# Kernel optimization log

Hardware: AMD Instinct MI355X
Metric: run time of the kernel (lower is better)

Reference implementation:

```python
import jax, jax.numpy as jnp
import numpy as np

K = 20  # neighbors per point (module default)


def _knn_idx(x, k):
    # x: [N, d] -> indices of k nearest points (self included, as in torch_cluster.knn)
    d2 = jnp.sum(x * x, axis=-1)
    dist = d2[:, None] + d2[None, :] - 2.0 * (x @ x.T)  # [N, N] squared distances
    _, idx = jax.lax.top_k(-dist, k)  # smallest distances
    return idx  # [N, k]


def _mlp(h, layers):
    # layers: list of (W, b, relu_flag); BN is identity (eval mode, fresh running stats)
    for W, b, relu in layers:
        h = h @ W + b
        if relu:
            h = jax.nn.relu(h)
    return h


def _dynamic_edge_conv(x, layers, k=K):
    # x: [B, N, d]; dynamic kNN graph per graph, edge feat [x_i, x_j - x_i], MLP, max-aggr
    idx = jax.vmap(lambda xx: _knn_idx(jax.lax.stop_gradient(xx), k))(x)  # [B, N, k]
    xj = jax.vmap(lambda xx, ii: xx[ii])(x, idx)  # [B, N, k, d] neighbor gather
    xi = x[:, :, None, :]
    feat = jnp.concatenate([jnp.broadcast_to(xi, xj.shape), xj - xi], axis=-1)  # [B,N,k,2d]
    return jnp.max(_mlp(feat, layers), axis=2)  # [B, N, d_out]


def setup_inputs() -> dict:
    key = jax.random.key(0)
    ks = jax.random.split(key, 20)
    s = 0.05
    B, N, PD, OUT = 8, 4096, 2, 10
    f32 = jnp.float32

    def w(k, shape):
        return jax.random.normal(k, shape, dtype=f32) * s

    return {
        "data": jax.random.normal(ks[0], (B, N, PD), dtype=f32),
        # conv1 MLP: [2*PD, 64, 64, 64]
        "c1w1": w(ks[1], (2 * PD, 64)), "c1b1": jnp.zeros((64,), f32),
        "c1w2": w(ks[2], (64, 64)),     "c1b2": jnp.zeros((64,), f32),
        "c1w3": w(ks[3], (64, 64)),     "c1b3": jnp.zeros((64,), f32),
        # conv2 MLP: [2*64, 128]
        "c2w1": w(ks[4], (128, 128)),   "c2b1": jnp.zeros((128,), f32),
        # lin1: 192 -> 1024
        "lin1_w": w(ks[5], (192, 1024)), "lin1_b": jnp.zeros((1024,), f32),
        # head MLP: [1024, 512, 256, OUT]
        "mw1": w(ks[6], (1024, 512)), "mb1": jnp.zeros((512,), f32),
        "mw2": w(ks[7], (512, 256)),  "mb2": jnp.zeros((256,), f32),
        "mw3": w(ks[8], (256, OUT)),  "mb3": jnp.zeros((OUT,), f32),
    }


def reference(data, c1w1, c1b1, c1w2, c1b2, c1w3, c1b3, c2w1, c2b1,
              lin1_w, lin1_b, mw1, mb1, mw2, mb2, mw3, mb3):
    # DynamicEdgeConv 1: MLP([4,64,64,64]) (plain last layer)
    x1 = _dynamic_edge_conv(data, [(c1w1, c1b1, True), (c1w2, c1b2, True), (c1w3, c1b3, False)])
    # DynamicEdgeConv 2: MLP([128,128]) (single plain linear)
    x2 = _dynamic_edge_conv(x1, [(c2w1, c2b1, False)])
    out = jnp.concatenate([x1, x2], axis=-1) @ lin1_w + lin1_b  # [B, N, 1024]
    out = jnp.max(out, axis=1)  # global max pool over points -> [B, 1024]
    out = _mlp(out, [(mw1, mb1, True), (mw2, mb2, True), (mw3, mb3, False)])
    return jax.nn.log_softmax(out, axis=1)
```

## Files before the change

### kernel.cpp

```cpp
#include <hip/hip_runtime.h>
#include <math.h>

#define DEVI static __device__ __forceinline__
#define F_INF __builtin_inff()

DEVI bool lexlt(float d, int i, float dr, int ir)
{
    return (d < dr) || (d == dr && i < ir);
}

DEVI void insert20(float* bd, int* bi, float d, int i)
{
#pragma unroll
    for (int j = 19; j >= 1; --j) {
        bool lt  = d < bd[j];
        bool ltp = d < bd[j - 1];
        float nd = ltp ? bd[j - 1] : d;
        int   ni = ltp ? bi[j - 1] : i;
        bd[j] = lt ? nd : bd[j];
        bi[j] = lt ? ni : bi[j];
    }
    bool lt0 = d < bd[0];
    bd[0] = lt0 ? d : bd[0];
    bi[0] = lt0 ? i : bi[0];
}

DEVI void insert_tiered(float* bd, int* bi, float d, int i)
{
    if (__all(!(d < bd[15]))) {
#pragma unroll
        for (int j = 19; j >= 17; --j) {
            bool lt  = d < bd[j];
            bool ltp = d < bd[j - 1];
            float nd = ltp ? bd[j - 1] : d;
            int   ni = ltp ? bi[j - 1] : i;
            bd[j] = lt ? nd : bd[j];
            bi[j] = lt ? ni : bi[j];
        }
        bool lt16 = d < bd[16];
        bd[16] = lt16 ? d : bd[16];
        bi[16] = lt16 ? i : bi[16];
    } else if (__all(!(d < bd[7]))) {
#pragma unroll
        for (int j = 19; j >= 9; --j) {
            bool lt  = d < bd[j];
            bool ltp = d < bd[j - 1];
            float nd = ltp ? bd[j - 1] : d;
            int   ni = ltp ? bi[j - 1] : i;
            bd[j] = lt ? nd : bd[j];
            bi[j] = lt ? ni : bi[j];
        }
        bool lt8 = d < bd[8];
        bd[8] = lt8 ? d : bd[8];
        bi[8] = lt8 ? i : bi[8];
    } else {
        insert20(bd, bi, d, i);
    }
}

DEVI void flushT(float* bd, int* bi, float d, int i, int e, int cnt)
{
    bool want = (e < cnt) && (d < bd[19]);
    if (__any(want))
        insert_tiered(bd, bi, want ? d : F_INF, want ? i : 0x7FFFFFFF);
}

#define FLUSH() do { \
    flushT(bd, bi, a0, j0, 0, cnt); \
    flushT(bd, bi, a1, j1, 1, cnt); \
    flushT(bd, bi, a2, j2, 2, cnt); \
    flushT(bd, bi, a3, j3, 3, cnt); \
    cnt = 0; thr = bd[19]; \
} while (0)

#define APPEND(dv, civ) do { \
    bool pass_ = (dv) < thr; \
    if (pass_) { \
        a0 = (cnt == 0) ? (dv) : a0; j0 = (cnt == 0) ? (civ) : j0; \
        a1 = (cnt == 1) ? (dv) : a1; j1 = (cnt == 1) ? (civ) : j1; \
        a2 = (cnt == 2) ? (dv) : a2; j2 = (cnt == 2) ? (civ) : j2; \
        a3 = (cnt == 3) ? (dv) : a3; j3 = (cnt == 3) ? (civ) : j3; \
        ++cnt; \
    } \
    if (__any(cnt == 4)) { FLUSH(); } \
} while (0)

__global__ __launch_bounds__(256) void k_merge8(const float* __restrict__ partD,
                                                const int* __restrict__ partI,
                                                int* __restrict__ idxo)
{
    int q = blockIdx.x * 256 + threadIdx.x;
    const float* rd = partD + (size_t)q * 160;
    const int*   ri = partI + (size_t)q * 160;
    int p0 = 0, p1 = 0, p2 = 0, p3 = 0, p4 = 0, p5 = 0, p6 = 0, p7 = 0;
    int* op = idxo + (size_t)q * 20;
    for (int r = 0; r < 20; ++r) {
        float d0 = rd[p0],        d1 = rd[20 + p1];
        float d2v = rd[40 + p2],  d3 = rd[60 + p3];
        float d4 = rd[80 + p4],   d5 = rd[100 + p5];
        float d6 = rd[120 + p6],  d7 = rd[140 + p7];
        int   i0 = ri[p0],        i1 = ri[20 + p1];
        int   i2 = ri[40 + p2],   i3 = ri[60 + p3];
        int   i4v = ri[80 + p4],  i5 = ri[100 + p5];
        int   i6 = ri[120 + p6],  i7 = ri[140 + p7];
        bool wA = lexlt(d1, i1, d0, i0);   float dA = wA ? d1 : d0; int iA = wA ? i1 : i0; int sA = wA ? 1 : 0;
        bool wB = lexlt(d3, i3, d2v, i2);  float dB = wB ? d3 : d2v; int iB = wB ? i3 : i2; int sB = wB ? 3 : 2;
        bool wC = lexlt(d5, i5, d4, i4v);  float dC = wC ? d5 : d4; int iC = wC ? i5 : i4v; int sC = wC ? 5 : 4;
        bool wD = lexlt(d7, i7, d6, i6);   float dD = wD ? d7 : d6; int iD = wD ? i7 : i6; int sD = wD ? 7 : 6;
        bool wE = lexlt(dB, iB, dA, iA);   float dE = wE ? dB : dA; int iE = wE ? iB : iA; int sE = wE ? sB : sA;
        bool wF = lexlt(dD, iD, dC, iC);   float dF = wF ? dD : dC; int iF = wF ? iD : iC; int sF = wF ? sD : sC;
        bool wG = lexlt(dF, iF, dE, iE);   int ig = wG ? iF : iE;   int sg = wG ? sF : sE;
        op[r] = ig;
        p0 += (sg == 0); p1 += (sg == 1); p2 += (sg == 2); p3 += (sg == 3);
        p4 += (sg == 4); p5 += (sg == 5); p6 += (sg == 6); p7 += (sg == 7);
    }
}

__global__ __launch_bounds__(256, 4) void k_knn2d(const float* __restrict__ x,
                                                  float* __restrict__ partD, int* __restrict__ partI)
{
    __shared__ float2 pts[4096];
    int t = threadIdx.x;
    int blk = blockIdx.x;
    int b = blk >> 7;
    int qt = (blk >> 1) & 63;
    int s = blk & 1;
    const float* xb = x + (size_t)b * 4096 * 2;
    for (int f = t; f < 2048; f += 256)
        ((float4*)pts)[f] = ((const float4*)xb)[f];
    __syncthreads();

    int l = t & 63, w = t >> 6;
    int q = qt * 64 + l;
    float2 qp = pts[q];
    float d2i = qp.x * qp.x + qp.y * qp.y;

    float bd[20]; int bi[20];
#pragma unroll
    for (int j = 0; j < 20; ++j) { bd[j] = F_INF; bi[j] = -1; }
    int cnt = 0; float thr = F_INF;
    float a0 = 0, a1 = 0, a2 = 0, a3 = 0;
    int   j0 = 0, j1 = 0, j2 = 0, j3 = 0;

    int m0 = s * 2048 + w * 512;
    for (int m = m0; m < m0 + 512; ++m) {
        float2 p = pts[m];
        float d2j = p.x * p.x + p.y * p.y;
        float dot = qp.x * p.x + qp.y * p.y;
        float dist = (d2i + d2j) - 2.0f * dot;
        APPEND(dist, m);
    }
    FLUSH();

    size_t base = (((size_t)(b * 4096 + q)) * 8 + s * 4 + w) * 20;
#pragma unroll
    for (int k = 0; k < 20; ++k) { partD[base + k] = bd[k]; partI[base + k] = bi[k]; }
}

__global__ void k_prep1(const float* __restrict__ x, const float* __restrict__ w1,
                        const float* __restrict__ b1, float* __restrict__ pm, float* __restrict__ qv)
{
    int tid = blockIdx.x * 256 + threadIdx.x;
    int n = tid >> 6, i = tid & 63;
    float x0 = x[(size_t)n * 2], x1v = x[(size_t)n * 2 + 1];
    float wa = w1[i], wb = w1[64 + i], wc = w1[128 + i], wd = w1[192 + i];
    pm[tid] = fmaf(x0, wa - wc, fmaf(x1v, wb - wd, b1[i]));
    qv[tid] = fmaf(x0, wc, x1v * wd);
}

__global__ __launch_bounds__(256) void k_edge1(const float* __restrict__ pm, const float* __restrict__ q,
                                               const int* __restrict__ idx1,
                                               const float* __restrict__ w2, const float* __restrict__ b2,
                                               const float* __restrict__ w3, const float* __restrict__ b3,
                                               float* __restrict__ x1, float* __restrict__ d2x1)
{
    int t = threadIdx.x;
    int w = t >> 6, l = t & 63;
    int pg = l / 20;
    int k  = l - pg * 20;
    int n0 = blockIdx.x * 12 + w * 3 + pg;
    bool valid = (l < 60) && (n0 < 32768);
    int n = valid ? n0 : 0;
    int b = n >> 12;
    int j = idx1[(size_t)n * 20 + k];
    const float4* pmr = (const float4*)(pm + (size_t)n * 64);
    const float4* qr  = (const float4*)(q + ((size_t)(b * 4096) + j) * 64);

    float h1[64];
#pragma unroll
    for (int i4 = 0; i4 < 16; ++i4) {
        float4 a = pmr[i4], c = qr[i4];
        h1[i4 * 4 + 0] = fmaxf(a.x + c.x, 0.f);
        h1[i4 * 4 + 1] = fmaxf(a.y + c.y, 0.f);
        h1[i4 * 4 + 2] = fmaxf(a.z + c.z, 0.f);
        h1[i4 * 4 + 3] = fmaxf(a.w + c.w, 0.f);
    }
    float h2[64];
#pragma unroll
    for (int o = 0; o < 64; ++o) h2[o] = b2[o];
#pragma unroll
    for (int i = 0; i < 64; ++i) {
        const float* r = w2 + i * 64;
#pragma unroll
        for (int o = 0; o < 64; ++o) h2[o] = fmaf(h1[i], r[o], h2[o]);
    }
#pragma unroll
    for (int o = 0; o < 64; ++o) h2[o] = fmaxf(h2[o], 0.f);

    float h3[64];
#pragma unroll
    for (int o = 0; o < 64; ++o) h3[o] = b3[o];
#pragma unroll
    for (int i = 0; i < 64; ++i) {
        const float* r = w3 + i * 64;
#pragma unroll
        for (int o = 0; o < 64; ++o) h3[o] = fmaf(h2[i], r[o], h3[o]);
    }

    int s16 = (k + 16 < 20) ? (l + 16) : l;
    int s8  = (k + 8  < 20) ? (l + 8)  : l;
    int s4  = (k + 4  < 20) ? (l + 4)  : l;
    int s2  = (k + 2  < 20) ? (l + 2)  : l;
    int s1  = (k + 1  < 20) ? (l + 1)  : l;
#pragma unroll
    for (int o = 0; o < 64; ++o) {
        float v = h3[o];
        v = fmaxf(v, __shfl(v, s16));
        v = fmaxf(v, __shfl(v, s8));
        v = fmaxf(v, __shfl(v, s4));
        v = fmaxf(v, __shfl(v, s2));
        v = fmaxf(v, __shfl(v, s1));
        h3[o] = v;
    }
    if (valid && k == 0) {
        float d2 = 0.f;
#pragma unroll
        for (int o = 0; o < 64; ++o) d2 += h3[o] * h3[o];
        float4* op = (float4*)(x1 + (size_t)n * 64);
#pragma unroll
        for (int i4 = 0; i4 < 16; ++i4)
            op[i4] = make_float4(h3[i4 * 4], h3[i4 * 4 + 1], h3[i4 * 4 + 2], h3[i4 * 4 + 3]);
        d2x1[n] = d2;
    }
}

#define S68 68
__global__ __launch_bounds__(256, 4) void k_knn64(const float* __restrict__ x1,
                                                  const float* __restrict__ d2x1,
                                                  float* __restrict__ partD, int* __restrict__ partI)
{
    __shared__ float smem[2 * 64 * S68 + 128];
    float* Qs   = smem;
    float* Cs   = smem + 64 * S68;
    float* d2q  = smem + 2 * 64 * S68;
    float* d2cs = d2q + 64;

    int t  = threadIdx.x;
    int blk = blockIdx.x;
    int bb = blk >> 7;
    int qt = (blk >> 1) & 63;
    int s  = blk & 1;
    int qbase  = bb * 4096 + qt * 64;
    int cstart = s * 2048;

    for (int f = t; f < 1024; f += 256) {
        int qq = f >> 4, dp = f & 15;
        *(float4*)&Qs[qq * S68 + dp * 4] =
            *(const float4*)(x1 + ((size_t)(qbase + qq)) * 64 + dp * 4);
    }
    if (t < 64) d2q[t] = d2x1[qbase + t];
    __syncthreads();

    int w = t >> 6, l = t & 63;
    int m = l & 15, p = l >> 4;
    float* Crow = Cs + (16 * w) * S68;

    float bd[20]; int bi[20];
#pragma unroll
    for (int j = 0; j < 20; ++j) { bd[j] = F_INF; bi[j] = -1; }
    int cnt = 0; float thr = F_INF;
    float a0 = 0, a1 = 0, a2 = 0, a3 = 0;
    int   j0 = 0, j1 = 0, j2 = 0, j3 = 0;

    float d2qr[4];
#pragma unroll
    for (int i = 0; i < 4; ++i) d2qr[i] = d2q[m + 16 * i];

    for (int T = 0; T < 32; ++T) {
        int cg = bb * 4096 + cstart + T * 64 + 16 * w;

#pragma unroll
        for (int r = 0; r < 4; ++r) {
            int rl = 4 * r + p;
            *(float4*)&Crow[rl * S68 + m * 4] =
                *(const float4*)(x1 + ((size_t)(cg + rl)) * 64 + m * 4);
        }
        if (l < 16) d2cs[16 * w + l] = d2x1[cg + l];

        float acc[4][4];
#pragma unroll
        for (int i = 0; i < 4; ++i)
#pragma unroll
            for (int j = 0; j < 4; ++j) acc[i][j] = 0.f;
#pragma unroll
        for (int dc = 0; dc < 16; ++dc) {
            float4 qv[4], cv[4];
#pragma unroll
            for (int i = 0; i < 4; ++i) qv[i] = *(const float4*)&Qs[(m + 16 * i) * S68 + dc * 4];
#pragma unroll
            for (int j = 0; j < 4; ++j) cv[j] = *(const float4*)&Crow[(4 * p + j) * S68 + dc * 4];
#pragma unroll
            for (int i = 0; i < 4; ++i)
#pragma unroll
                for (int j = 0; j < 4; ++j) {
                    acc[i][j] = fmaf(qv[i].x, cv[j].x, acc[i][j]);
                    acc[i][j] = fmaf(qv[i].y, cv[j].y, acc[i][j]);
                    acc[i][j] = fmaf(qv[i].z, cv[j].z, acc[i][j]);
                    acc[i][j] = fmaf(qv[i].w, cv[j].w, acc[i][j]);
                }
        }
        float d2cr[4];
#pragma unroll
        for (int j = 0; j < 4; ++j) d2cr[j] = d2cs[16 * w + 4 * p + j];

#pragma unroll
        for (int j = 0; j < 4; ++j)
#pragma unroll
            for (int i = 0; i < 4; ++i)
                Crow[(4 * p + j) * S68 + (m + 16 * i)] =
                    (d2qr[i] + d2cr[j]) - 2.0f * acc[i][j];

        int cib = cstart + T * 64 + 16 * w;
#pragma unroll
        for (int c = 0; c < 16; ++c) {
            float dv = Crow[c * S68 + l];
            APPEND(dv, cib + c);
        }
    }
    FLUSH();

    size_t base = (((size_t)(qbase + l)) * 8 + s * 4 + w) * 20;
#pragma unroll
    for (int k = 0; k < 20; ++k) { partD[base + k] = bd[k]; partI[base + k] = bi[k]; }
}

__global__ __launch_bounds__(128) void k_prep2(const float* __restrict__ x1, const float* __restrict__ w,
                                               const float* __restrict__ bias,
                                               float* __restrict__ T, float* __restrict__ V)
{
    __shared__ float xs[8][64];
    int o = threadIdx.x;
    int g = blockIdx.x * 8;
    for (int t = threadIdx.x; t < 512; t += 128) xs[t >> 6][t & 63] = x1[(size_t)g * 64 + t];
    __syncthreads();
    float at[8] = {}, av[8] = {};
    for (int i = 0; i < 64; ++i) {
        float wt = w[i * 128 + o], wv = w[(64 + i) * 128 + o];
#pragma unroll
        for (int p = 0; p < 8; ++p) {
            float xv = xs[p][i];
            at[p] = fmaf(xv, wt, at[p]);
            av[p] = fmaf(xv, wv, av[p]);
        }
    }
    float bo = bias[o];
#pragma unroll
    for (int p = 0; p < 8; ++p) {
        T[(size_t)(g + p) * 128 + o] = at[p] - av[p] + bo;
        V[(size_t)(g + p) * 128 + o] = av[p];
    }
}

__global__ __launch_bounds__(256) void k_edge2(const float* __restrict__ T, const float* __restrict__ V,
                                               const int* __restrict__ idx2, float* __restrict__ x2)
{
    int t = threadIdx.x;
    int p = t >> 5, oc = t & 31;
    int n = blockIdx.x * 8 + p;
    int b = n >> 12;
    const int* ip = idx2 + (size_t)n * 20;
    float4 mx = make_float4(-F_INF, -F_INF, -F_INF, -F_INF);
    for (int k = 0; k < 20; ++k) {
        int j = ip[k];
        float4 v = ((const float4*)(V + ((size_t)(b * 4096) + j) * 128))[oc];
        mx.x = fmaxf(mx.x, v.x); mx.y = fmaxf(mx.y, v.y);
        mx.z = fmaxf(mx.z, v.z); mx.w = fmaxf(mx.w, v.w);
    }
    float4 tv = ((const float4*)(T + (size_t)n * 128))[oc];
    float4 r = make_float4(tv.x + mx.x, tv.y + mx.y, tv.z + mx.z, tv.w + mx.w);
    ((float4*)(x2 + (size_t)n * 128))[oc] = r;
}

__global__ __launch_bounds__(256) void k_lin1max(const float* __restrict__ x1, const float* __restrict__ x2,
                                                 const float* __restrict__ w, const float* __restrict__ bias,
                                                 float* __restrict__ partial)
{
    __shared__ float fs[32][192];
    int blk = blockIdx.x;
    int b = blk >> 7, c = blk & 127;
    int base_n = b * 4096 + c * 32;
    for (int t = threadIdx.x; t < 2048; t += 256) {
        int n = t >> 6, i = t & 63;
        fs[n][i] = x1[(size_t)(base_n + n) * 64 + i];
    }
    for (int t = threadIdx.x; t < 4096; t += 256) {
        int n = t >> 7, i = t & 127;
        fs[n][64 + i] = x2[(size_t)(base_n + n) * 128 + i];
    }
    __syncthreads();

    float acc[32][4];
#pragma unroll
    for (int n = 0; n < 32; ++n)
#pragma unroll
        for (int oo = 0; oo < 4; ++oo) acc[n][oo] = 0.f;

    for (int i4 = 0; i4 < 48; ++i4) {
        float wv[4][4];
#pragma unroll
        for (int r = 0; r < 4; ++r)
#pragma unroll
            for (int oo = 0; oo < 4; ++oo)
                wv[r][oo] = w[(size_t)(i4 * 4 + r) * 1024 + oo * 256 + threadIdx.x];
#pragma unroll
        for (int n = 0; n < 32; ++n) {
            float4 f = *(const float4*)&fs[n][i4 * 4];
#pragma unroll
            for (int oo = 0; oo < 4; ++oo) {
                acc[n][oo] = fmaf(f.x, wv[0][oo], acc[n][oo]);
                acc[n][oo] = fmaf(f.y, wv[1][oo], acc[n][oo]);
                acc[n][oo] = fmaf(f.z, wv[2][oo], acc[n][oo]);
                acc[n][oo] = fmaf(f.w, wv[3][oo], acc[n][oo]);
            }
        }
    }
#pragma unroll
    for (int oo = 0; oo < 4; ++oo) {
        int o = oo * 256 + threadIdx.x;
        float m = -F_INF;
#pragma unroll
        for (int n = 0; n < 32; ++n) m = fmaxf(m, acc[n][oo]);
        partial[((size_t)b * 128 + c) * 1024 + o] = m + bias[o];
    }
}

__global__ void k_red(const float* __restrict__ partial, float* __restrict__ pooled)
{
    int t = blockIdx.x * 256 + threadIdx.x;
    int b = t >> 10, o = t & 1023;
    float m = -F_INF;
    for (int c = 0; c < 128; ++c) m = fmaxf(m, partial[((size_t)b * 128 + c) * 1024 + o]);
    pooled[t] = m;
}

__global__ __launch_bounds__(256) void k_fc1(const float* __restrict__ pooled, const float* __restrict__ w,
                                             const float* __restrict__ bias, float* __restrict__ g1)
{
    __shared__ float ps[8 * 1024];
    for (int t = threadIdx.x; t < 8192; t += 256) ps[t] = pooled[t];
    __syncthreads();
    int o = blockIdx.x * 256 + threadIdx.x;
    float acc[8] = {};
    for (int i4 = 0; i4 < 256; ++i4) {
        float w0 = w[(size_t)(i4 * 4 + 0) * 512 + o];
        float w1v = w[(size_t)(i4 * 4 + 1) * 512 + o];
        float w2v = w[(size_t)(i4 * 4 + 2) * 512 + o];
        float w3v = w[(size_t)(i4 * 4 + 3) * 512 + o];
#pragma unroll
        for (int bb = 0; bb < 8; ++bb) {
            float4 f = *(const float4*)&ps[bb * 1024 + i4 * 4];
            acc[bb] = fmaf(f.x, w0, fmaf(f.y, w1v, fmaf(f.z, w2v, fmaf(f.w, w3v, acc[bb]))));
        }
    }
    float bo = bias[o];
#pragma unroll
    for (int bb = 0; bb < 8; ++bb) g1[bb * 512 + o] = fmaxf(acc[bb] + bo, 0.f);
}

__global__ __launch_bounds__(256) void k_fc2(const float* __restrict__ g1, const float* __restrict__ w,
                                             const float* __restrict__ bias, float* __restrict__ g2)
{
    __shared__ float gs[8 * 512];
    for (int t = threadIdx.x; t < 4096; t += 256) gs[t] = g1[t];
    __syncthreads();
    int o = threadIdx.x;
    float acc[8] = {};
    for (int i4 = 0; i4 < 128; ++i4) {
        float w0 = w[(size_t)(i4 * 4 + 0) * 256 + o];
        float w1v = w[(size_t)(i4 * 4 + 1) * 256 + o];
        float w2v = w[(size_t)(i4 * 4 + 2) * 256 + o];
        float w3v = w[(size_t)(i4 * 4 + 3) * 256 + o];
#pragma unroll
        for (int bb = 0; bb < 8; ++bb) {
            float4 f = *(const float4*)&gs[bb * 512 + i4 * 4];
            acc[bb] = fmaf(f.x, w0, fmaf(f.y, w1v, fmaf(f.z, w2v, fmaf(f.w, w3v, acc[bb]))));
        }
    }
    float bo = bias[o];
#pragma unroll
    for (int bb = 0; bb < 8; ++bb) g2[bb * 256 + o] = fmaxf(acc[bb] + bo, 0.f);
}

__global__ void k_fc3sm(const float* __restrict__ g2, const float* __restrict__ w,
                        const float* __restrict__ bias, float* __restrict__ out)
{
    int t = threadIdx.x;
    int b = t >> 4, l = t & 15;
    float lg = -F_INF;
    if (l < 10) {
        float a = bias[l];
        for (int i = 0; i < 256; ++i) a = fmaf(g2[b * 256 + i], w[i * 10 + l], a);
        lg = a;
    }
    float m = lg;
    m = fmaxf(m, __shfl_xor(m, 1, 16));
    m = fmaxf(m, __shfl_xor(m, 2, 16));
    m = fmaxf(m, __shfl_xor(m, 4, 16));
    m = fmaxf(m, __shfl_xor(m, 8, 16));
    float e = (l < 10) ? expf(lg - m) : 0.f;
    float s = e;
    s += __shfl_xor(s, 1, 16);
    s += __shfl_xor(s, 2, 16);
    s += __shfl_xor(s, 4, 16);
    s += __shfl_xor(s, 8, 16);
    if (l < 10) out[b * 10 + l] = (lg - m) - logf(s);
}

extern "C" void kernel_launch(void* const* d_in, const int* in_sizes, int n_in,
                              void* d_out, int out_size, void* d_ws, size_t ws_size,
                              hipStream_t stream)
{
    (void)in_sizes; (void)n_in; (void)out_size; (void)ws_size;
    const float* data  = (const float*)d_in[0];
    const float* c1w1  = (const float*)d_in[1];
    const float* c1b1  = (const float*)d_in[2];
    const float* c1w2  = (const float*)d_in[3];
    const float* c1b2  = (const float*)d_in[4];
    const float* c1w3  = (const float*)d_in[5];
    const float* c1b3  = (const float*)d_in[6];
    const float* c2w1  = (const float*)d_in[7];
    const float* c2b1  = (const float*)d_in[8];
    const float* lin1w = (const float*)d_in[9];
    const float* lin1b = (const float*)d_in[10];
    const float* mw1   = (const float*)d_in[11];
    const float* mb1   = (const float*)d_in[12];
    const float* mw2   = (const float*)d_in[13];
    const float* mb2   = (const float*)d_in[14];
    const float* mw3   = (const float*)d_in[15];
    const float* mb3   = (const float*)d_in[16];
    float* ws  = (float*)d_ws;
    int*   wsi = (int*)d_ws;
    float* out = (float*)d_out;

    const size_t OFF_IDX1 = 0;
    const size_t OFF_IDX2 = 0;
    const size_t OFF_X1   = 655360;
    const size_t OFF_D2   = 2752512;
    const size_t OFF_PM   = 2785280;
    const size_t OFF_Q    = 4882432;
    const size_t OFF_PD   = 2785280;
    const size_t OFF_PI   = 8028160;
    const size_t OFF_T    = 2785280;
    const size_t OFF_V    = 6979584;
    const size_t OFF_X2   = 11173888;
    const size_t OFF_PART = 15368192;
    const size_t OFF_POOL = 16416768;
    const size_t OFF_G1   = 16424960;
    const size_t OFF_G2   = 16429056;

    k_knn2d<<<1024, 256, 0, stream>>>(data, ws + OFF_PD, wsi + OFF_PI);
    k_merge8<<<128, 256, 0, stream>>>(ws + OFF_PD, wsi + OFF_PI, wsi + OFF_IDX1);
    k_prep1<<<8192, 256, 0, stream>>>(data, c1w1, c1b1, ws + OFF_PM, ws + OFF_Q);
    k_edge1<<<2731, 256, 0, stream>>>(ws + OFF_PM, ws + OFF_Q, wsi + OFF_IDX1,
                                      c1w2, c1b2, c1w3, c1b3, ws + OFF_X1, ws + OFF_D2);
    k_knn64<<<1024, 256, 0, stream>>>(ws + OFF_X1, ws + OFF_D2, ws + OFF_PD, wsi + OFF_PI);
    k_merge8<<<128, 256, 0, stream>>>(ws + OFF_PD, wsi + OFF_PI, wsi + OFF_IDX2);
    k_prep2<<<4096, 128, 0, stream>>>(ws + OFF_X1, c2w1, c2b1, ws + OFF_T, ws + OFF_V);
    k_edge2<<<4096, 256, 0, stream>>>(ws + OFF_T, ws + OFF_V, wsi + OFF_IDX2, ws + OFF_X2);
    k_lin1max<<<1024, 256, 0, stream>>>(ws + OFF_X1, ws + OFF_X2, lin1w, lin1b, ws + OFF_PART);
    k_red<<<32, 256, 0, stream>>>(ws + OFF_PART, ws + OFF_POOL);
    k_fc1<<<2, 256, 0, stream>>>(ws + OFF_POOL, mw1, mb1, ws + OFF_G1);
    k_fc2<<<1, 256, 0, stream>>>(ws + OFF_G1, mw2, mb2, ws + OFF_G2);
    k_fc3sm<<<1, 128, 0, stream>>>(ws + OFF_G2, mw3, mb3, out);
}
```

Measured before the change: 1.445 ms.

## Hold query rows in registers and stream candidates as scalar loads in knn64

The 64-dim kNN kernel drops the shared-memory register-tiled 4x4 dot-product micro-kernel. Each thread now keeps its own query row in 64 registers and reads each candidate row through a wave-uniform (readfirstlane) pointer, so candidate data comes in as scalar/broadcast loads with no LDS staging or distance transpose. This removes the LDS traffic and the shared scratch, but puts much higher register pressure on each thread and gives up the 4x4 reuse of loaded operands. The merge kernel also moves from 256-thread to 64-thread blocks, giving more blocks for the same query count.

```diff
diff --git a/kernel.cpp b/kernel.cpp
--- a/kernel.cpp
+++ b/kernel.cpp
@@ -85,11 +85,11 @@
     if (__any(cnt == 4)) { FLUSH(); } \
 } while (0)
 
-__global__ __launch_bounds__(256) void k_merge8(const float* __restrict__ partD,
-                                                const int* __restrict__ partI,
-                                                int* __restrict__ idxo)
-{
-    int q = blockIdx.x * 256 + threadIdx.x;
+__global__ __launch_bounds__(64) void k_merge8(const float* __restrict__ partD,
+                                               const int* __restrict__ partI,
+                                               int* __restrict__ idxo)
+{
+    int q = blockIdx.x * 64 + threadIdx.x;
     const float* rd = partD + (size_t)q * 160;
     const int*   ri = partI + (size_t)q * 160;
     int p0 = 0, p1 = 0, p2 = 0, p3 = 0, p4 = 0, p5 = 0, p6 = 0, p7 = 0;
@@ -244,17 +244,10 @@
     }
 }
 
-#define S68 68
-__global__ __launch_bounds__(256, 4) void k_knn64(const float* __restrict__ x1,
-                                                  const float* __restrict__ d2x1,
-                                                  float* __restrict__ partD, int* __restrict__ partI)
-{
-    __shared__ float smem[2 * 64 * S68 + 128];
-    float* Qs   = smem;
-    float* Cs   = smem + 64 * S68;
-    float* d2q  = smem + 2 * 64 * S68;
-    float* d2cs = d2q + 64;
-
+__global__ __launch_bounds__(256) void k_knn64(const float* __restrict__ x1,
+                                               const float* __restrict__ d2x1,
+                                               float* __restrict__ partD, int* __restrict__ partI)
+{
     int t  = threadIdx.x;
     int blk = blockIdx.x;
     int bb = blk >> 7;
@@ -262,18 +255,17 @@
     int s  = blk & 1;
     int qbase  = bb * 4096 + qt * 64;
     int cstart = s * 2048;
-
-    for (int f = t; f < 1024; f += 256) {
-        int qq = f >> 4, dp = f & 15;
-        *(float4*)&Qs[qq * S68 + dp * 4] =
-            *(const float4*)(x1 + ((size_t)(qbase + qq)) * 64 + dp * 4);
-    }
-    if (t < 64) d2q[t] = d2x1[qbase + t];
-    __syncthreads();
-
     int w = t >> 6, l = t & 63;
-    int m = l & 15, p = l >> 4;
-    float* Crow = Cs + (16 * w) * S68;
+
+    float qreg[64];
+    const float4* qp = (const float4*)(x1 + (size_t)(qbase + l) * 64);
+#pragma unroll
+    for (int i4 = 0; i4 < 16; ++i4) {
+        float4 v = qp[i4];
+        qreg[i4 * 4 + 0] = v.x; qreg[i4 * 4 + 1] = v.y;
+        qreg[i4 * 4 + 2] = v.z; qreg[i4 * 4 + 3] = v.w;
+    }
+    float d2ql = d2x1[qbase + l];
 
     float bd[20]; int bi[20];
 #pragma unroll
@@ -282,59 +274,21 @@
     float a0 = 0, a1 = 0, a2 = 0, a3 = 0;
     int   j0 = 0, j1 = 0, j2 = 0, j3 = 0;
 
-    float d2qr[4];
-#pragma unroll
-    for (int i = 0; i < 4; ++i) d2qr[i] = d2q[m + 16 * i];
+    int cg0 = bb * 4096 + cstart + 16 * w;
 
     for (int T = 0; T < 32; ++T) {
-        int cg = bb * 4096 + cstart + T * 64 + 16 * w;
-
-#pragma unroll
-        for (int r = 0; r < 4; ++r) {
-            int rl = 4 * r + p;
-            *(float4*)&Crow[rl * S68 + m * 4] =
-                *(const float4*)(x1 + ((size_t)(cg + rl)) * 64 + m * 4);
-        }
-        if (l < 16) d2cs[16 * w + l] = d2x1[cg + l];
-
-        float acc[4][4];
-#pragma unroll
-        for (int i = 0; i < 4; ++i)
-#pragma unroll
-            for (int j = 0; j < 4; ++j) acc[i][j] = 0.f;
-#pragma unroll
-        for (int dc = 0; dc < 16; ++dc) {
-            float4 qv[4], cv[4];
-#pragma unroll
-            for (int i = 0; i < 4; ++i) qv[i] = *(const float4*)&Qs[(m + 16 * i) * S68 + dc * 4];
-#pragma unroll
-            for (int j = 0; j < 4; ++j) cv[j] = *(const float4*)&Crow[(4 * p + j) * S68 + dc * 4];
-#pragma unroll
-            for (int i = 0; i < 4; ++i)
-#pragma unroll
-                for (int j = 0; j < 4; ++j) {
-                    acc[i][j] = fmaf(qv[i].x, cv[j].x, acc[i][j]);
-                    acc[i][j] = fmaf(qv[i].y, cv[j].y, acc[i][j]);
-                    acc[i][j] = fmaf(qv[i].z, cv[j].z, acc[i][j]);
-                    acc[i][j] = fmaf(qv[i].w, cv[j].w, acc[i][j]);
-                }
-        }
-        float d2cr[4];
-#pragma unroll
-        for (int j = 0; j < 4; ++j) d2cr[j] = d2cs[16 * w + 4 * p + j];
-
-#pragma unroll
-        for (int j = 0; j < 4; ++j)
-#pragma unroll
-            for (int i = 0; i < 4; ++i)
-                Crow[(4 * p + j) * S68 + (m + 16 * i)] =
-                    (d2qr[i] + d2cr[j]) - 2.0f * acc[i][j];
-
-        int cib = cstart + T * 64 + 16 * w;
-#pragma unroll
-        for (int c = 0; c < 16; ++c) {
-            float dv = Crow[c * S68 + l];
-            APPEND(dv, cib + c);
+        int cg = cg0 + T * 64;
+#pragma unroll
+        for (int j = 0; j < 16; ++j) {
+            int cu = __builtin_amdgcn_readfirstlane(cg + j);
+            const float* __restrict__ cr = x1 + (size_t)cu * 64;
+            float d2c = d2x1[cu];
+            float dot = 0.f;
+#pragma unroll
+            for (int d = 0; d < 64; ++d)
+                dot = fmaf(qreg[d], cr[d], dot);
+            float dist = (d2ql + d2c) - 2.0f * dot;
+            APPEND(dist, cstart + T * 64 + 16 * w + j);
         }
     }
     FLUSH();
@@ -569,12 +523,12 @@
     const size_t OFF_G2   = 16429056;
 
     k_knn2d<<<1024, 256, 0, stream>>>(data, ws + OFF_PD, wsi + OFF_PI);
-    k_merge8<<<128, 256, 0, stream>>>(ws + OFF_PD, wsi + OFF_PI, wsi + OFF_IDX1);
+    k_merge8<<<512, 64, 0, stream>>>(ws + OFF_PD, wsi + OFF_PI, wsi + OFF_IDX1);
     k_prep1<<<8192, 256, 0, stream>>>(data, c1w1, c1b1, ws + OFF_PM, ws + OFF_Q);
     k_edge1<<<2731, 256, 0, stream>>>(ws + OFF_PM, ws + OFF_Q, wsi + OFF_IDX1,
                                       c1w2, c1b2, c1w3, c1b3, ws + OFF_X1, ws + OFF_D2);
     k_knn64<<<1024, 256, 0, stream>>>(ws + OFF_X1, ws + OFF_D2, ws + OFF_PD, wsi + OFF_PI);
-    k_merge8<<<128, 256, 0, stream>>>(ws + OFF_PD, wsi + OFF_PI, wsi + OFF_IDX2);
+    k_merge8<<<512, 64, 0, stream>>>(ws + OFF_PD, wsi + OFF_PI, wsi + OFF_IDX2);
     k_prep2<<<4096, 128, 0, stream>>>(ws + OFF_X1, c2w1, c2b1, ws + OFF_T, ws + OFF_V);
     k_edge2<<<4096, 256, 0, stream>>>(ws + OFF_T, ws + OFF_V, wsi + OFF_IDX2, ws + OFF_X2);
     k_lin1max<<<1024, 256, 0, stream>>>(ws + OFF_X1, ws + OFF_X2, lin1w, lin1b, ws + OFF_PART);
```

Result: slower. 2.258 ms (+56.3%).
